# Kernel tuning notes

Measured on AMD Instinct MI355X. Metric: run time of the kernel, lower is better.

Reference implementation:

```python
import jax, jax.numpy as jnp
import numpy as np

B, N, FE, T, OUT = 32, 2048, 32, 12, 3


def setup_inputs() -> dict:
    key = jax.random.key(0)
    ks = jax.random.split(key, 7)
    return {
        "x": jax.random.normal(ks[0], (B, N, FE, T), dtype=jnp.float32),
        "w_ih": jax.random.normal(ks[1], (3, FE), dtype=jnp.float32) * 0.1,
        "w_hh": jax.random.normal(ks[2], (3, 1), dtype=jnp.float32) * 0.1,
        "b_ih": jax.random.normal(ks[3], (3,), dtype=jnp.float32) * 0.1,
        "b_hh": jax.random.normal(ks[4], (3,), dtype=jnp.float32) * 0.1,
        "lin_w": jax.random.normal(ks[5], (OUT, T), dtype=jnp.float32) * 0.1,
        "lin_b": jax.random.normal(ks[6], (OUT,), dtype=jnp.float32) * 0.1,
        "unused": 0,
    }


def reference(x, w_ih, w_hh, b_ih, b_hh, lin_w, lin_b, unused):
    b, n, fe, t = x.shape
    # [B,N,Fe,T] -> [M,T,Fe] with M = B*N
    xs = jnp.transpose(x.reshape(-1, fe, t), (0, 2, 1))
    # Precompute input-to-gate projections for all timesteps: [M,T,3] (r,z,n gates)
    gates_x = jnp.einsum("mtf,gf->mtg", xs, w_ih) + b_ih
    wh = w_hh[:, 0]  # [3] recurrent weights, hidden size is 1

    def step(h, gx):
        # h: [M], gx: [M,3]
        r = jax.nn.sigmoid(gx[:, 0] + wh[0] * h + b_hh[0])
        z = jax.nn.sigmoid(gx[:, 1] + wh[1] * h + b_hh[1])
        nn_ = jnp.tanh(gx[:, 2] + r * (wh[2] * h + b_hh[2]))
        h_new = (1.0 - z) * nn_ + z * h
        return h_new, h_new

    h0 = jnp.zeros(xs.shape[0], dtype=x.dtype)
    _, hs = jax.lax.scan(step, h0, jnp.swapaxes(gates_x, 0, 1))  # [T,M]
    h = jax.nn.relu(hs.T)  # [M,T] (squeeze of [M,T,1])
    out = h @ lin_w.T + lin_b  # [M,OUT]
    return out.reshape(b, n, -1)
```

## Files before the change

kernel.cpp:

```cpp
#include <hip/hip_runtime.h>

#define FE_ 32
#define T_  12
#define M_  (32 * 2048)
#define SEQ_PER_BLOCK 32
#define THREADS (SEQ_PER_BLOCK * T_)
#define LDS_STRIDE 37

__global__ __launch_bounds__(THREADS) void gru_fused_kernel(
    const float* __restrict__ x,
    const float* __restrict__ w_ih,
    const float* __restrict__ w_hh,
    const float* __restrict__ b_ih,
    const float* __restrict__ b_hh,
    const float* __restrict__ lin_w,
    const float* __restrict__ lin_b,
    float* __restrict__ out)
{
    __shared__ float gbuf[SEQ_PER_BLOCK * LDS_STRIDE];

    const int tid = threadIdx.x;
    const int s   = tid / T_;
    const int t   = tid - s * T_;
    const int m0  = blockIdx.x * SEQ_PER_BLOCK;

    const float* __restrict__ xp = x + (size_t)(m0 + s) * (FE_ * T_) + t;
    float a0 = b_ih[0], a1 = b_ih[1], a2 = b_ih[2];
#pragma unroll
    for (int f = 0; f < FE_; ++f) {
        const float xv = xp[f * T_];
        a0 = fmaf(xv, w_ih[0 * FE_ + f], a0);
        a1 = fmaf(xv, w_ih[1 * FE_ + f], a1);
        a2 = fmaf(xv, w_ih[2 * FE_ + f], a2);
    }
    float* g = &gbuf[s * LDS_STRIDE + t * 3];
    g[0] = a0; g[1] = a1; g[2] = a2;
    __syncthreads();

    if (tid < SEQ_PER_BLOCK) {
        const float wh0 = w_hh[0], wh1 = w_hh[1], wh2 = w_hh[2];
        const float bh0 = b_hh[0], bh1 = b_hh[1], bh2 = b_hh[2];
        float o0 = lin_b[0], o1 = lin_b[1], o2 = lin_b[2];
        const float* __restrict__ gg = &gbuf[tid * LDS_STRIDE];
        float h = 0.0f;
#pragma unroll
        for (int tt = 0; tt < T_; ++tt) {
            const float r = 1.0f / (1.0f + __expf(-(gg[tt * 3 + 0] + wh0 * h + bh0)));
            const float z = 1.0f / (1.0f + __expf(-(gg[tt * 3 + 1] + wh1 * h + bh1)));
            const float y = gg[tt * 3 + 2] + r * (wh2 * h + bh2);
            const float n = 1.0f - 2.0f / (1.0f + __expf(2.0f * y));
            h = (1.0f - z) * n + z * h;
            const float ht = h > 0.0f ? h : 0.0f;
            o0 = fmaf(ht, lin_w[0 * T_ + tt], o0);
            o1 = fmaf(ht, lin_w[1 * T_ + tt], o1);
            o2 = fmaf(ht, lin_w[2 * T_ + tt], o2);
        }
        float* __restrict__ po = out + (size_t)(m0 + tid) * 3;
        po[0] = o0; po[1] = o1; po[2] = o2;
    }
}

extern "C" void kernel_launch(void* const* d_in, const int* in_sizes, int n_in,
                              void* d_out, int out_size, void* d_ws, size_t ws_size,
                              hipStream_t stream) {
    (void)in_sizes; (void)n_in; (void)d_ws; (void)ws_size; (void)out_size;
    const float* x     = (const float*)d_in[0];
    const float* w_ih  = (const float*)d_in[1];
    const float* w_hh  = (const float*)d_in[2];
    const float* b_ih  = (const float*)d_in[3];
    const float* b_hh  = (const float*)d_in[4];
    const float* lin_w = (const float*)d_in[5];
    const float* lin_b = (const float*)d_in[6];
    float* out = (float*)d_out;

    const int grid = M_ / SEQ_PER_BLOCK;
    gru_fused_kernel<<<grid, THREADS, 0, stream>>>(x, w_ih, w_hh, b_ih, b_hh,
                                                   lin_w, lin_b, out);
}
```

Baseline: 159.0 us.

## Split each sequence across four lanes with float4 loads and shuffle-based recurrence

Each sequence is now handled by four lanes. Three of them load float4 chunks of timesteps and compute the gate projections for four timesteps each. The recurrence is computed redundantly in all four lanes, with gate values passed by width-4 shuffles, and each lane accumulates one output channel. This removes the LDS staging buffer, the __syncthreads, and the serial single-thread recurrence that left most threads idle. In exchange the fourth lane duplicates lane 2's loads and work, and the shuffles are on the critical path of every timestep.

```diff
diff --git a/kernel.cpp b/kernel.cpp
--- a/kernel.cpp
+++ b/kernel.cpp
@@ -3,9 +3,9 @@
 #define FE_ 32
 #define T_  12
 #define M_  (32 * 2048)
-#define SEQ_PER_BLOCK 32
-#define THREADS (SEQ_PER_BLOCK * T_)
-#define LDS_STRIDE 37
+#define LANES_PER_SEQ 4
+#define SEQ_PER_BLOCK 64
+#define THREADS (SEQ_PER_BLOCK * LANES_PER_SEQ)
 
 __global__ __launch_bounds__(THREADS) void gru_fused_kernel(
     const float* __restrict__ x,
@@ -17,47 +17,72 @@
     const float* __restrict__ lin_b,
     float* __restrict__ out)
 {
-    __shared__ float gbuf[SEQ_PER_BLOCK * LDS_STRIDE];
+    const int tid = threadIdx.x;
+    const int q   = tid & 3;
+    const int s   = tid >> 2;
+    const int m   = blockIdx.x * SEQ_PER_BLOCK + s;
+    const int p   = (q < 3) ? q : 2;
 
-    const int tid = threadIdx.x;
-    const int s   = tid / T_;
-    const int t   = tid - s * T_;
-    const int m0  = blockIdx.x * SEQ_PER_BLOCK;
+    const float4* __restrict__ xp =
+        reinterpret_cast<const float4*>(x + (size_t)m * (FE_ * T_)) + p;
 
-    const float* __restrict__ xp = x + (size_t)(m0 + s) * (FE_ * T_) + t;
-    float a0 = b_ih[0], a1 = b_ih[1], a2 = b_ih[2];
+    const float bi0 = b_ih[0], bi1 = b_ih[1], bi2 = b_ih[2];
+    float a0[4], a1[4], a2[4];
+#pragma unroll
+    for (int j = 0; j < 4; ++j) { a0[j] = bi0; a1[j] = bi1; a2[j] = bi2; }
+
 #pragma unroll
     for (int f = 0; f < FE_; ++f) {
-        const float xv = xp[f * T_];
-        a0 = fmaf(xv, w_ih[0 * FE_ + f], a0);
-        a1 = fmaf(xv, w_ih[1 * FE_ + f], a1);
-        a2 = fmaf(xv, w_ih[2 * FE_ + f], a2);
+        const float4 xv = xp[f * 3];
+        const float w0 = w_ih[0 * FE_ + f];
+        const float w1 = w_ih[1 * FE_ + f];
+        const float w2 = w_ih[2 * FE_ + f];
+        a0[0] = fmaf(xv.x, w0, a0[0]);
+        a0[1] = fmaf(xv.y, w0, a0[1]);
+        a0[2] = fmaf(xv.z, w0, a0[2]);
+        a0[3] = fmaf(xv.w, w0, a0[3]);
+        a1[0] = fmaf(xv.x, w1, a1[0]);
+        a1[1] = fmaf(xv.y, w1, a1[1]);
+        a1[2] = fmaf(xv.z, w1, a1[2]);
+        a1[3] = fmaf(xv.w, w1, a1[3]);
+        a2[0] = fmaf(xv.x, w2, a2[0]);
+        a2[1] = fmaf(xv.y, w2, a2[1]);
+        a2[2] = fmaf(xv.z, w2, a2[2]);
+        a2[3] = fmaf(xv.w, w2, a2[3]);
     }
-    float* g = &gbuf[s * LDS_STRIDE + t * 3];
-    g[0] = a0; g[1] = a1; g[2] = a2;
-    __syncthreads();
 
-    if (tid < SEQ_PER_BLOCK) {
-        const float wh0 = w_hh[0], wh1 = w_hh[1], wh2 = w_hh[2];
-        const float bh0 = b_hh[0], bh1 = b_hh[1], bh2 = b_hh[2];
-        float o0 = lin_b[0], o1 = lin_b[1], o2 = lin_b[2];
-        const float* __restrict__ gg = &gbuf[tid * LDS_STRIDE];
-        float h = 0.0f;
+    const float wh0 = w_hh[0], wh1 = w_hh[1], wh2 = w_hh[2];
+    const float bh0 = b_hh[0], bh1 = b_hh[1], bh2 = b_hh[2];
+
+    const int qe = (q < 3) ? q : 2;
+    const float4* __restrict__ lw4 =
+        reinterpret_cast<const float4*>(lin_w + qe * T_);
+    const float4 lwa = lw4[0], lwb = lw4[1], lwc = lw4[2];
+    const float lw[12] = { lwa.x, lwa.y, lwa.z, lwa.w,
+                           lwb.x, lwb.y, lwb.z, lwb.w,
+                           lwc.x, lwc.y, lwc.z, lwc.w };
+
+    float oq = lin_b[qe];
+    float h  = 0.0f;
 #pragma unroll
-        for (int tt = 0; tt < T_; ++tt) {
-            const float r = 1.0f / (1.0f + __expf(-(gg[tt * 3 + 0] + wh0 * h + bh0)));
-            const float z = 1.0f / (1.0f + __expf(-(gg[tt * 3 + 1] + wh1 * h + bh1)));
-            const float y = gg[tt * 3 + 2] + r * (wh2 * h + bh2);
-            const float n = 1.0f - 2.0f / (1.0f + __expf(2.0f * y));
-            h = (1.0f - z) * n + z * h;
-            const float ht = h > 0.0f ? h : 0.0f;
-            o0 = fmaf(ht, lin_w[0 * T_ + tt], o0);
-            o1 = fmaf(ht, lin_w[1 * T_ + tt], o1);
-            o2 = fmaf(ht, lin_w[2 * T_ + tt], o2);
-        }
-        float* __restrict__ po = out + (size_t)(m0 + tid) * 3;
-        po[0] = o0; po[1] = o1; po[2] = o2;
+    for (int tt = 0; tt < T_; ++tt) {
+        const int d  = tt >> 2;
+        const int j  = tt & 3;
+        const float g0 = __shfl(a0[j], d, LANES_PER_SEQ);
+        const float g1 = __shfl(a1[j], d, LANES_PER_SEQ);
+        const float g2 = __shfl(a2[j], d, LANES_PER_SEQ);
+
+        const float r = 1.0f / (1.0f + __expf(-(g0 + wh0 * h + bh0)));
+        const float z = 1.0f / (1.0f + __expf(-(g1 + wh1 * h + bh1)));
+        const float y = g2 + r * (wh2 * h + bh2);
+        const float n = 1.0f - 2.0f / (1.0f + __expf(2.0f * y));
+        h = (1.0f - z) * n + z * h;
+
+        const float ht = h > 0.0f ? h : 0.0f;
+        oq = fmaf(ht, lw[tt], oq);
     }
+
+    if (q < 3) out[(size_t)m * 3 + q] = oq;
 }
 
 extern "C" void kernel_launch(void* const* d_in, const int* in_sizes, int n_in,
```

After: 158.9 us. About the same (-0.1%).
